# Performance work log

Measured on AMD Instinct MI355X. Metric: run time of the kernel, lower is better.

The kernel has to match this reference:

```python
import jax, jax.numpy as jnp
import numpy as np

DEPTH = 8
INPUT_DIM = 256
OUTPUT_DIM = 32
BATCH = 131072
N_INNER = 2 ** DEPTH - 1   # 255 inner nodes in heap/level order
N_LEAF = 2 ** DEPTH        # 256 leaves


def setup_inputs() -> dict:
    key = jax.random.key(0)
    kx, kw, kb, kbeta, kleaf = jax.random.split(key, 5)
    x = jax.random.normal(kx, (BATCH, INPUT_DIM), dtype=jnp.float32)
    # Stacked per-node Linear(input_dim, 1): weight rows [N_INNER, INPUT_DIM], bias [N_INNER]
    W = jax.random.normal(kw, (N_INNER, INPUT_DIM), dtype=jnp.float32) / np.sqrt(INPUT_DIM)
    b = jax.random.normal(kb, (N_INNER,), dtype=jnp.float32) * 0.01
    beta = jax.random.normal(kbeta, (N_INNER,), dtype=jnp.float32)  # per-node beta scalar
    leaf_param = jax.random.normal(kleaf, (N_LEAF, OUTPUT_DIM), dtype=jnp.float32)
    return {"x": x, "W": W, "b": b, "beta": beta, "leaf_param": leaf_param}


def _soft_tree(x, W, b, beta, leaf_param):
    B = x.shape[0]
    # All inner-node splits in one GEMM: sigmoid(beta_n * (x @ w_n + b_n))
    prob = jax.nn.sigmoid(beta[None, :] * (x @ W.T + b[None, :]))  # [B, N_INNER]
    # Level-wise path probability propagation (nodes stored in heap/level order).
    p = jnp.ones((B, 1), dtype=x.dtype)
    for d in range(DEPTH):
        lo = 2 ** d - 1
        pr = prob[:, lo: lo + 2 ** d]                      # [B, 2^d]
        # left child gets p*pr, right child gets p*(1-pr); interleave to keep DFS order
        p = jnp.stack([p * pr, p * (1.0 - pr)], axis=-1).reshape(B, 2 ** (d + 1))
    # leaf distributions Q = softmax(param) broadcast over batch; mixture output
    Q = jax.nn.softmax(leaf_param, axis=-1)                # [N_LEAF, OUTPUT_DIM]
    out = p @ Q                                            # [B, OUTPUT_DIM]
    return out, p


def reference(x, W, b, beta, leaf_param):
    out, path_probs = _soft_tree(x, W, b, beta, leaf_param)
    return out, path_probs
```

## Files before the change

kernel.cpp:

```cpp
#include <hip/hip_runtime.h>

#define BATCH   131072
#define IN_DIM  256
#define OUT_DIM 32
#define N_INNER 255
#define N_LEAF  256
#define OUT_HDR (BATCH * OUT_DIM)

#define TILE_M  64
#define BK      32
#define NTHR    512
#define NCHUNK  8
#define PSTR    258
#define INV64K  (1.0f / 65536.0f)

#define WS_QT_HI   0
#define WS_QT_LO   16384
#define WS_WIMG_HI 32768
#define WS_WIMG_LO (32768 + 131072)

#define L_XS_HI 0
#define L_XS_LO 4096
#define L_WS_HI 8192
#define L_WS_LO 24576
#define SMEM_BYTES 40960

typedef __attribute__((ext_vector_type(8))) short bf16x8;
typedef __attribute__((ext_vector_type(4))) float f32x4;

__device__ __forceinline__ unsigned short bf16rne(float a) {
    unsigned u = __float_as_uint(a);
    return (unsigned short)((u + 0x7FFFu + ((u >> 16) & 1u)) >> 16);
}
__device__ __forceinline__ unsigned packhi2(float a, float b) {
    return (unsigned)bf16rne(a) | ((unsigned)bf16rne(b) << 16);
}
__device__ __forceinline__ unsigned packlo2(float a, float b) {
    unsigned short ha = bf16rne(a), hb = bf16rne(b);
    float ra = a - __uint_as_float((unsigned)ha << 16);
    float rb = b - __uint_as_float((unsigned)hb << 16);
    return (unsigned)bf16rne(ra) | ((unsigned)bf16rne(rb) << 16);
}
__device__ __forceinline__ void split2(float a, float b, unsigned& hi, unsigned& lo) {
    unsigned short ha = bf16rne(a), hb = bf16rne(b);
    hi = (unsigned)ha | ((unsigned)hb << 16);
    float ra = a - __uint_as_float((unsigned)ha << 16);
    float rb = b - __uint_as_float((unsigned)hb << 16);
    lo = (unsigned)bf16rne(ra) | ((unsigned)bf16rne(rb) << 16);
}

__device__ __forceinline__ void gload16(const void* g, void* l) {
    __builtin_amdgcn_global_load_lds(
        (const __attribute__((address_space(1))) unsigned int*)g,
        (__attribute__((address_space(3))) unsigned int*)l, 16, 0, 0);
}

__global__ void wsplit_k(const float* __restrict__ W,
                         unsigned int* __restrict__ whi, unsigned int* __restrict__ wlo) {
    int gid = blockIdx.x * 512 + threadIdx.x;
    int n   = gid >> 5;
    int oct = gid & 31;
    float4 a = make_float4(0.f,0.f,0.f,0.f), b = a;
    if (n < N_INNER) {
        a = *(const float4*)(W + (size_t)n * IN_DIM + oct * 8);
        b = *(const float4*)(W + (size_t)n * IN_DIM + oct * 8 + 4);
    }
    uint4 h, l;
    split2(a.x, a.y, h.x, l.x); split2(a.z, a.w, h.y, l.y);
    split2(b.x, b.y, h.z, l.z); split2(b.z, b.w, h.w, l.w);
    int c = oct >> 2, kg = oct & 3;
    size_t off = ((size_t)(c * 4 + kg) * 256 + n) * 4;
    *(uint4*)(whi + off) = h;
    *(uint4*)(wlo + off) = l;
}

__global__ void qt_k(const float* __restrict__ leaf,
                     unsigned short* __restrict__ qhi, unsigned short* __restrict__ qlo) {
    int l = threadIdx.x;
    const float* row = leaf + l * OUT_DIM;
    float v[OUT_DIM];
    float mx = -1e30f;
#pragma unroll
    for (int o = 0; o < OUT_DIM; ++o) { v[o] = row[o]; mx = fmaxf(mx, v[o]); }
    float s = 0.f;
#pragma unroll
    for (int o = 0; o < OUT_DIM; ++o) { v[o] = __expf(v[o] - mx); s += v[o]; }
    float r = 1.f / s;
#pragma unroll
    for (int o = 0; o < OUT_DIM; ++o) {
        float q = v[o] * r;
        unsigned short h = bf16rne(q);
        float res = q - __uint_as_float((unsigned)h << 16);
        qhi[o * 256 + l] = h;
        qlo[o * 256 + l] = bf16rne(res);
    }
}

#define TREE_STAGE(D) { \
    const int base_ = (1 << (D)) - 1 + (qq << ((D) - 3)); \
    _Pragma("unroll") \
    for (int i = (1 << ((D) - 3)) - 1; i >= 0; --i) { \
        float pr_ = (float)pb[base_ + i] * INV64K; \
        float a_  = P[i]; \
        float lv_ = a_ * pr_; \
        P[2*i]     = lv_; \
        P[2*i + 1] = a_ - lv_; \
    } }

#define MFMA_BF16(A, B, C) __builtin_amdgcn_mfma_f32_16x16x32_bf16(A, B, C, 0, 0, 0)

__launch_bounds__(NTHR, 6)
__global__ void tree_k(const float* __restrict__ x,
                       const float* __restrict__ bv, const float* __restrict__ beta,
                       const unsigned short* __restrict__ qhi, const unsigned short* __restrict__ qlo,
                       const char* __restrict__ wimg_hi, const char* __restrict__ wimg_lo,
                       float* __restrict__ out) {
    extern __shared__ char smem[];
    const int tid  = threadIdx.x;
    const int row0 = blockIdx.x * TILE_M;

    const int lane  = tid & 63;
    const int w     = tid >> 6;
    const int col16 = lane & 15;
    const int hi4   = lane >> 4;
    const int wr    = w >> 2;
    const int wc    = w & 3;

    f32x4 acc[2][4];
#pragma unroll
    for (int i = 0; i < 2; ++i)
#pragma unroll
        for (int j = 0; j < 4; ++j) acc[i][j] = (f32x4){0.f, 0.f, 0.f, 0.f};

    const int xrow = tid >> 3;
    const int xkq  = tid & 7;
    const int xoff = (xkq >> 1) * 1024 + xrow * 16 + (xkq & 1) * 8;
    const float* xsrc = x + (size_t)(row0 + xrow) * IN_DIM + xkq * 4;

#pragma unroll 1
    for (int c = 0; c < NCHUNK; ++c) {
        {
            const char* gh = wimg_hi + (size_t)c * 16384;
            const char* gl = wimg_lo + (size_t)c * 16384;
            char* dh = smem + L_WS_HI + w * 1024;
            char* dl = smem + L_WS_LO + w * 1024;
            gload16(gh + tid * 16,        dh);
            gload16(gh + 8192 + tid * 16, dh + 8192);
            gload16(gl + tid * 16,        dl);
            gload16(gl + 8192 + tid * 16, dl + 8192);
        }
        {
            float4 v = *(const float4*)(xsrc + c * BK);
            uint2 h, l;
            split2(v.x, v.y, h.x, l.x);
            split2(v.z, v.w, h.y, l.y);
            *(uint2*)(smem + L_XS_HI + xoff) = h;
            *(uint2*)(smem + L_XS_LO + xoff) = l;
        }
        __syncthreads();

        bf16x8 ah[2], al[2];
#pragma unroll
        for (int rf = 0; rf < 2; ++rf) {
            int ao = hi4 * 1024 + (wr * 32 + rf * 16 + col16) * 16;
            ah[rf] = *(const bf16x8*)(smem + L_XS_HI + ao);
            al[rf] = *(const bf16x8*)(smem + L_XS_LO + ao);
        }
#pragma unroll
        for (int cf = 0; cf < 4; ++cf) {
            int bo = hi4 * 4096 + (wc * 64 + cf * 16 + col16) * 16;
            bf16x8 bh = *(const bf16x8*)(smem + L_WS_HI + bo);
            bf16x8 bl = *(const bf16x8*)(smem + L_WS_LO + bo);
#pragma unroll
            for (int rf = 0; rf < 2; ++rf) {
                acc[rf][cf] = MFMA_BF16(ah[rf], bh, acc[rf][cf]);
                acc[rf][cf] = MFMA_BF16(ah[rf], bl, acc[rf][cf]);
                acc[rf][cf] = MFMA_BF16(al[rf], bh, acc[rf][cf]);
            }
        }
        __syncthreads();
    }

    unsigned short* prob = (unsigned short*)smem;
    {
        float bb[4], bt[4];
#pragma unroll
        for (int cf = 0; cf < 4; ++cf) {
            int col = wc * 64 + cf * 16 + col16;
            bb[cf] = (col < N_INNER) ? bv[col]   : 0.f;
            bt[cf] = (col < N_INNER) ? beta[col] : 0.f;
        }
#pragma unroll
        for (int rf = 0; rf < 2; ++rf)
#pragma unroll
            for (int cf = 0; cf < 4; ++cf) {
                int col = wc * 64 + cf * 16 + col16;
#pragma unroll
                for (int r = 0; r < 4; ++r) {
                    int row = wr * 32 + rf * 16 + hi4 * 4 + r;
                    float t = (acc[rf][cf][r] + bb[cf]) * bt[cf];
                    float s = 1.f / (1.f + __expf(-t));
                    float u = fminf(s * 65536.f + 0.5f, 65535.f);
                    prob[row * PSTR + col] = (unsigned short)(unsigned)u;
                }
            }
    }
    __syncthreads();

    const int prow = tid >> 3;
    const int qq   = tid & 7;
    const unsigned short* pb = prob + prow * PSTR;
    float P[32];
    {
        float p0 = (float)pb[0] * INV64K;             float f0 = (qq & 4) ? (1.f - p0) : p0;
        float p1 = (float)pb[1 + (qq >> 2)] * INV64K; float f1 = (qq & 2) ? (1.f - p1) : p1;
        float p2 = (float)pb[3 + (qq >> 1)] * INV64K; float f2 = (qq & 1) ? (1.f - p2) : p2;
        P[0] = f0 * f1 * f2;
    }
    TREE_STAGE(3) TREE_STAGE(4) TREE_STAGE(5) TREE_STAGE(6) TREE_STAGE(7)

    {
        float* po = out + OUT_HDR + (size_t)(row0 + prow) * N_LEAF + qq * 32;
#pragma unroll
        for (int m = 0; m < 8; ++m)
            *(float4*)(po + m * 4) = make_float4(P[4*m], P[4*m+1], P[4*m+2], P[4*m+3]);
    }
    __syncthreads();

#pragma unroll
    for (int kg = 0; kg < 4; ++kg) {
        uint4 h;
        h.x = packhi2(P[kg*8+0], P[kg*8+1]);
        h.y = packhi2(P[kg*8+2], P[kg*8+3]);
        h.z = packhi2(P[kg*8+4], P[kg*8+5]);
        h.w = packhi2(P[kg*8+6], P[kg*8+7]);
        *(uint4*)(smem + qq * 4096 + kg * 1024 + ((prow * 16) ^ (qq << 4))) = h;
    }
    __syncthreads();

    f32x4 acc2 = (f32x4){0.f,0.f,0.f,0.f};
    const int cfw  = w >> 2;
    const int arow = (w & 3) * 16 + col16;
    const int qcol = (cfw * 16 + col16) * 256;

#pragma unroll
    for (int kc = 0; kc < 8; ++kc) {
        bf16x8 pa = *(const bf16x8*)(smem + kc * 4096 + hi4 * 1024 + ((arow * 16) ^ (kc << 4)));
        int qo = qcol + kc * 32 + hi4 * 8;
        bf16x8 qbh = *(const bf16x8*)(qhi + qo);
        bf16x8 qbl = *(const bf16x8*)(qlo + qo);
        acc2 = MFMA_BF16(pa, qbh, acc2);
        acc2 = MFMA_BF16(pa, qbl, acc2);
    }
    __syncthreads();

#pragma unroll
    for (int kg = 0; kg < 4; ++kg) {
        uint4 l;
        l.x = packlo2(P[kg*8+0], P[kg*8+1]);
        l.y = packlo2(P[kg*8+2], P[kg*8+3]);
        l.z = packlo2(P[kg*8+4], P[kg*8+5]);
        l.w = packlo2(P[kg*8+6], P[kg*8+7]);
        *(uint4*)(smem + qq * 4096 + kg * 1024 + ((prow * 16) ^ (qq << 4))) = l;
    }
    __syncthreads();

#pragma unroll
    for (int kc = 0; kc < 8; ++kc) {
        bf16x8 pa = *(const bf16x8*)(smem + kc * 4096 + hi4 * 1024 + ((arow * 16) ^ (kc << 4)));
        int qo = qcol + kc * 32 + hi4 * 8;
        bf16x8 qbh = *(const bf16x8*)(qhi + qo);
        acc2 = MFMA_BF16(pa, qbh, acc2);
    }
#pragma unroll
    for (int r = 0; r < 4; ++r) {
        int row = (w & 3) * 16 + hi4 * 4 + r;
        out[(size_t)(row0 + row) * OUT_DIM + cfw * 16 + col16] = acc2[r];
    }
}

extern "C" void kernel_launch(void* const* d_in, const int* in_sizes, int n_in,
                              void* d_out, int out_size, void* d_ws, size_t ws_size,
                              hipStream_t stream) {
    const float* x    = (const float*)d_in[0];
    const float* W    = (const float*)d_in[1];
    const float* bv   = (const float*)d_in[2];
    const float* beta = (const float*)d_in[3];
    const float* leaf = (const float*)d_in[4];
    float* out = (float*)d_out;
    char* ws = (char*)d_ws;

    unsigned short* qhi = (unsigned short*)(ws + WS_QT_HI);
    unsigned short* qlo = (unsigned short*)(ws + WS_QT_LO);
    char* whi = ws + WS_WIMG_HI;
    char* wlo = ws + WS_WIMG_LO;

    hipFuncSetAttribute(reinterpret_cast<const void*>(tree_k),
                        hipFuncAttributeMaxDynamicSharedMemorySize, SMEM_BYTES);

    wsplit_k<<<16, 512, 0, stream>>>(W, (unsigned int*)whi, (unsigned int*)wlo);
    qt_k<<<1, 256, 0, stream>>>(leaf, qhi, qlo);
    tree_k<<<BATCH / TILE_M, NTHR, SMEM_BYTES, stream>>>(
        x, bv, beta, qhi, qlo, whi, wlo, out);
}
```

Measured before the change: 151.9 us.

## Load GEMM operands directly to registers and split both P images before the Q GEMM

```diff
diff --git a/kernel.cpp b/kernel.cpp
--- a/kernel.cpp
+++ b/kernel.cpp
@@ -11,7 +11,7 @@
 #define BK      32
 #define NTHR    512
 #define NCHUNK  8
-#define PSTR    258
+#define PSTR    260
 #define INV64K  (1.0f / 65536.0f)
 
 #define WS_QT_HI   0
@@ -19,11 +19,8 @@
 #define WS_WIMG_HI 32768
 #define WS_WIMG_LO (32768 + 131072)
 
-#define L_XS_HI 0
-#define L_XS_LO 4096
-#define L_WS_HI 8192
-#define L_WS_LO 24576
-#define SMEM_BYTES 40960
+#define IMG_LO     33792
+#define SMEM_BYTES (IMG_LO + 32768)
 
 typedef __attribute__((ext_vector_type(8))) short bf16x8;
 typedef __attribute__((ext_vector_type(4))) float f32x4;
@@ -49,10 +46,21 @@
     lo = (unsigned)bf16rne(ra) | ((unsigned)bf16rne(rb) << 16);
 }
 
-__device__ __forceinline__ void gload16(const void* g, void* l) {
-    __builtin_amdgcn_global_load_lds(
-        (const __attribute__((address_space(1))) unsigned int*)g,
-        (__attribute__((address_space(3))) unsigned int*)l, 16, 0, 0);
+__device__ __forceinline__ void tsplit2(float a, float b, unsigned& h, unsigned& l) {
+    unsigned ua = __float_as_uint(a), ub = __float_as_uint(b);
+    h = (ua >> 16) | (ub & 0xFFFF0000u);
+    float ra = a - __uint_as_float(ua & 0xFFFF0000u);
+    float rb = b - __uint_as_float(ub & 0xFFFF0000u);
+    l = (__float_as_uint(ra) >> 16) | (__float_as_uint(rb) & 0xFFFF0000u);
+}
+__device__ __forceinline__ void split8(float4 a, float4 b, bf16x8& h8, bf16x8& l8) {
+    uint4 h, l;
+    tsplit2(a.x, a.y, h.x, l.x);
+    tsplit2(a.z, a.w, h.y, l.y);
+    tsplit2(b.x, b.y, h.z, l.z);
+    tsplit2(b.z, b.w, h.w, l.w);
+    h8 = __builtin_bit_cast(bf16x8, h);
+    l8 = __builtin_bit_cast(bf16x8, l);
 }
 
 __global__ void wsplit_k(const float* __restrict__ W,
@@ -68,8 +76,8 @@
     uint4 h, l;
     split2(a.x, a.y, h.x, l.x); split2(a.z, a.w, h.y, l.y);
     split2(b.x, b.y, h.z, l.z); split2(b.z, b.w, h.w, l.w);
-    int c = oct >> 2, kg = oct & 3;
-    size_t off = ((size_t)(c * 4 + kg) * 256 + n) * 4;
+    int c = oct >> 2, koct = oct & 3;
+    size_t off = (size_t)c * 4096 + (size_t)n * 16 + koct * 4;
     *(uint4*)(whi + off) = h;
     *(uint4*)(wlo + off) = l;
 }
@@ -109,7 +117,7 @@
 
 #define MFMA_BF16(A, B, C) __builtin_amdgcn_mfma_f32_16x16x32_bf16(A, B, C, 0, 0, 0)
 
-__launch_bounds__(NTHR, 6)
+__launch_bounds__(NTHR, 4)
 __global__ void tree_k(const float* __restrict__ x,
                        const float* __restrict__ bv, const float* __restrict__ beta,
                        const unsigned short* __restrict__ qhi, const unsigned short* __restrict__ qlo,
@@ -132,53 +140,43 @@
 #pragma unroll
         for (int j = 0; j < 4; ++j) acc[i][j] = (f32x4){0.f, 0.f, 0.f, 0.f};
 
-    const int xrow = tid >> 3;
-    const int xkq  = tid & 7;
-    const int xoff = (xkq >> 1) * 1024 + xrow * 16 + (xkq & 1) * 8;
-    const float* xsrc = x + (size_t)(row0 + xrow) * IN_DIM + xkq * 4;
+    const float* xp0 = x + (size_t)(row0 + wr * 32 + col16) * IN_DIM + hi4 * 8;
+    const float* xp1 = xp0 + (size_t)16 * IN_DIM;
+    const int bbase = (wc * 64 + col16) * 64 + hi4 * 16;
+
+    float4 a00 = *(const float4*)(xp0);
+    float4 a01 = *(const float4*)(xp0 + 4);
+    float4 a10 = *(const float4*)(xp1);
+    float4 a11 = *(const float4*)(xp1 + 4);
 
 #pragma unroll 1
     for (int c = 0; c < NCHUNK; ++c) {
-        {
-            const char* gh = wimg_hi + (size_t)c * 16384;
-            const char* gl = wimg_lo + (size_t)c * 16384;
-            char* dh = smem + L_WS_HI + w * 1024;
-            char* dl = smem + L_WS_LO + w * 1024;
-            gload16(gh + tid * 16,        dh);
-            gload16(gh + 8192 + tid * 16, dh + 8192);
-            gload16(gl + tid * 16,        dl);
-            gload16(gl + 8192 + tid * 16, dl + 8192);
-        }
-        {
-            float4 v = *(const float4*)(xsrc + c * BK);
-            uint2 h, l;
-            split2(v.x, v.y, h.x, l.x);
-            split2(v.z, v.w, h.y, l.y);
-            *(uint2*)(smem + L_XS_HI + xoff) = h;
-            *(uint2*)(smem + L_XS_LO + xoff) = l;
-        }
-        __syncthreads();
-
-        bf16x8 ah[2], al[2];
-#pragma unroll
-        for (int rf = 0; rf < 2; ++rf) {
-            int ao = hi4 * 1024 + (wr * 32 + rf * 16 + col16) * 16;
-            ah[rf] = *(const bf16x8*)(smem + L_XS_HI + ao);
-            al[rf] = *(const bf16x8*)(smem + L_XS_LO + ao);
-        }
+        const char* bhp = wimg_hi + (size_t)c * 16384 + bbase;
+        const char* blp = wimg_lo + (size_t)c * 16384 + bbase;
+        bf16x8 bh[4], bl[4];
 #pragma unroll
         for (int cf = 0; cf < 4; ++cf) {
-            int bo = hi4 * 4096 + (wc * 64 + cf * 16 + col16) * 16;
-            bf16x8 bh = *(const bf16x8*)(smem + L_WS_HI + bo);
-            bf16x8 bl = *(const bf16x8*)(smem + L_WS_LO + bo);
-#pragma unroll
-            for (int rf = 0; rf < 2; ++rf) {
-                acc[rf][cf] = MFMA_BF16(ah[rf], bh, acc[rf][cf]);
-                acc[rf][cf] = MFMA_BF16(ah[rf], bl, acc[rf][cf]);
-                acc[rf][cf] = MFMA_BF16(al[rf], bh, acc[rf][cf]);
-            }
-        }
-        __syncthreads();
+            bh[cf] = *(const bf16x8*)(bhp + cf * 1024);
+            bl[cf] = *(const bf16x8*)(blp + cf * 1024);
+        }
+        bf16x8 ah0, al0, ah1, al1;
+        split8(a00, a01, ah0, al0);
+        split8(a10, a11, ah1, al1);
+        if (c + 1 < NCHUNK) {
+            a00 = *(const float4*)(xp0 + (c + 1) * BK);
+            a01 = *(const float4*)(xp0 + (c + 1) * BK + 4);
+            a10 = *(const float4*)(xp1 + (c + 1) * BK);
+            a11 = *(const float4*)(xp1 + (c + 1) * BK + 4);
+        }
+#pragma unroll
+        for (int cf = 0; cf < 4; ++cf) {
+            acc[0][cf] = MFMA_BF16(ah0, bh[cf], acc[0][cf]);
+            acc[1][cf] = MFMA_BF16(ah1, bh[cf], acc[1][cf]);
+            acc[0][cf] = MFMA_BF16(ah0, bl[cf], acc[0][cf]);
+            acc[1][cf] = MFMA_BF16(ah1, bl[cf], acc[1][cf]);
+            acc[0][cf] = MFMA_BF16(al0, bh[cf], acc[0][cf]);
+            acc[1][cf] = MFMA_BF16(al1, bh[cf], acc[1][cf]);
+        }
     }
 
     unsigned short* prob = (unsigned short*)smem;
@@ -225,6 +223,16 @@
         for (int m = 0; m < 8; ++m)
             *(float4*)(po + m * 4) = make_float4(P[4*m], P[4*m+1], P[4*m+2], P[4*m+3]);
     }
+
+#pragma unroll
+    for (int kg = 0; kg < 4; ++kg) {
+        uint4 l;
+        l.x = packlo2(P[kg*8+0], P[kg*8+1]);
+        l.y = packlo2(P[kg*8+2], P[kg*8+3]);
+        l.z = packlo2(P[kg*8+4], P[kg*8+5]);
+        l.w = packlo2(P[kg*8+6], P[kg*8+7]);
+        *(uint4*)(smem + IMG_LO + qq * 4096 + kg * 1024 + ((prow * 16) ^ (qq << 4))) = l;
+    }
     __syncthreads();
 
 #pragma unroll
@@ -245,32 +253,15 @@
 
 #pragma unroll
     for (int kc = 0; kc < 8; ++kc) {
-        bf16x8 pa = *(const bf16x8*)(smem + kc * 4096 + hi4 * 1024 + ((arow * 16) ^ (kc << 4)));
+        const int po = kc * 4096 + hi4 * 1024 + ((arow * 16) ^ (kc << 4));
+        bf16x8 ph = *(const bf16x8*)(smem + po);
+        bf16x8 pl = *(const bf16x8*)(smem + IMG_LO + po);
         int qo = qcol + kc * 32 + hi4 * 8;
         bf16x8 qbh = *(const bf16x8*)(qhi + qo);
         bf16x8 qbl = *(const bf16x8*)(qlo + qo);
-        acc2 = MFMA_BF16(pa, qbh, acc2);
-        acc2 = MFMA_BF16(pa, qbl, acc2);
-    }
-    __syncthreads();
-
-#pragma unroll
-    for (int kg = 0; kg < 4; ++kg) {
-        uint4 l;
-        l.x = packlo2(P[kg*8+0], P[kg*8+1]);
-        l.y = packlo2(P[kg*8+2], P[kg*8+3]);
-        l.z = packlo2(P[kg*8+4], P[kg*8+5]);
-        l.w = packlo2(P[kg*8+6], P[kg*8+7]);
-        *(uint4*)(smem + qq * 4096 + kg * 1024 + ((prow * 16) ^ (qq << 4))) = l;
-    }
-    __syncthreads();
-
-#pragma unroll
-    for (int kc = 0; kc < 8; ++kc) {
-        bf16x8 pa = *(const bf16x8*)(smem + kc * 4096 + hi4 * 1024 + ((arow * 16) ^ (kc << 4)));
-        int qo = qcol + kc * 32 + hi4 * 8;
-        bf16x8 qbh = *(const bf16x8*)(qhi + qo);
-        acc2 = MFMA_BF16(pa, qbh, acc2);
+        acc2 = MFMA_BF16(ph, qbh, acc2);
+        acc2 = MFMA_BF16(ph, qbl, acc2);
+        acc2 = MFMA_BF16(pl, qbh, acc2);
     }
 #pragma unroll
     for (int r = 0; r < 4; ++r) {
```

Result: slower. 200.6 us (+32.0%).

## Double-buffer GEMM chunks, truncate-split x, and merge hi/lo leaf-mixture passes

Applied to the files above, without the earlier changes.

```diff
diff --git a/kernel.cpp b/kernel.cpp
--- a/kernel.cpp
+++ b/kernel.cpp
@@ -11,7 +11,7 @@
 #define BK      32
 #define NTHR    512
 #define NCHUNK  8
-#define PSTR    258
+#define PSTR    260
 #define INV64K  (1.0f / 65536.0f)
 
 #define WS_QT_HI   0
@@ -19,11 +19,12 @@
 #define WS_WIMG_HI 32768
 #define WS_WIMG_LO (32768 + 131072)
 
-#define L_XS_HI 0
-#define L_XS_LO 4096
-#define L_WS_HI 8192
-#define L_WS_LO 24576
-#define SMEM_BYTES 40960
+#define WB0 0
+#define WB1 32768
+#define XB0 65536
+#define XB1 73728
+#define IMG_LO 34816
+#define SMEM_BYTES 81920
 
 typedef __attribute__((ext_vector_type(8))) short bf16x8;
 typedef __attribute__((ext_vector_type(4))) float f32x4;
@@ -47,6 +48,13 @@
     float ra = a - __uint_as_float((unsigned)ha << 16);
     float rb = b - __uint_as_float((unsigned)hb << 16);
     lo = (unsigned)bf16rne(ra) | ((unsigned)bf16rne(rb) << 16);
+}
+__device__ __forceinline__ void tsplit2(float a, float b, unsigned& h, unsigned& l) {
+    unsigned ua = __float_as_uint(a), ub = __float_as_uint(b);
+    h = (ua >> 16) | (ub & 0xFFFF0000u);
+    float ra = a - __uint_as_float(ua & 0xFFFF0000u);
+    float rb = b - __uint_as_float(ub & 0xFFFF0000u);
+    l = (__float_as_uint(ra) >> 16) | (__float_as_uint(rb) & 0xFFFF0000u);
 }
 
 __device__ __forceinline__ void gload16(const void* g, void* l) {
@@ -109,7 +117,7 @@
 
 #define MFMA_BF16(A, B, C) __builtin_amdgcn_mfma_f32_16x16x32_bf16(A, B, C, 0, 0, 0)
 
-__launch_bounds__(NTHR, 6)
+__launch_bounds__(NTHR, 4)
 __global__ void tree_k(const float* __restrict__ x,
                        const float* __restrict__ bv, const float* __restrict__ beta,
                        const unsigned short* __restrict__ qhi, const unsigned short* __restrict__ qlo,
@@ -137,46 +145,70 @@
     const int xoff = (xkq >> 1) * 1024 + xrow * 16 + (xkq & 1) * 8;
     const float* xsrc = x + (size_t)(row0 + xrow) * IN_DIM + xkq * 4;
 
+    {
+        char* dh = smem + WB0 + w * 1024;
+        char* dl = dh + 16384;
+        gload16(wimg_hi + tid * 16,        dh);
+        gload16(wimg_hi + 8192 + tid * 16, dh + 8192);
+        gload16(wimg_lo + tid * 16,        dl);
+        gload16(wimg_lo + 8192 + tid * 16, dl + 8192);
+        float4 v = *(const float4*)(xsrc);
+        uint2 h, l;
+        tsplit2(v.x, v.y, h.x, l.x);
+        tsplit2(v.z, v.w, h.y, l.y);
+        *(uint2*)(smem + XB0 + xoff)        = h;
+        *(uint2*)(smem + XB0 + 4096 + xoff) = l;
+    }
+    __syncthreads();
+
 #pragma unroll 1
     for (int c = 0; c < NCHUNK; ++c) {
-        {
-            const char* gh = wimg_hi + (size_t)c * 16384;
-            const char* gl = wimg_lo + (size_t)c * 16384;
-            char* dh = smem + L_WS_HI + w * 1024;
-            char* dl = smem + L_WS_LO + w * 1024;
+        const int cur = c & 1;
+        const char* wb = smem + (cur ? WB1 : WB0);
+        const char* xb = smem + (cur ? XB1 : XB0);
+        char* wbn = smem + (cur ? WB0 : WB1);
+        char* xbn = smem + (cur ? XB0 : XB1);
+
+        float4 xn;
+        const bool more = (c + 1 < NCHUNK);
+        if (more) {
+            const char* gh = wimg_hi + (size_t)(c + 1) * 16384;
+            const char* gl = wimg_lo + (size_t)(c + 1) * 16384;
+            char* dh = wbn + w * 1024;
+            char* dl = dh + 16384;
             gload16(gh + tid * 16,        dh);
             gload16(gh + 8192 + tid * 16, dh + 8192);
             gload16(gl + tid * 16,        dl);
             gload16(gl + 8192 + tid * 16, dl + 8192);
-        }
-        {
-            float4 v = *(const float4*)(xsrc + c * BK);
-            uint2 h, l;
-            split2(v.x, v.y, h.x, l.x);
-            split2(v.z, v.w, h.y, l.y);
-            *(uint2*)(smem + L_XS_HI + xoff) = h;
-            *(uint2*)(smem + L_XS_LO + xoff) = l;
-        }
-        __syncthreads();
+            xn = *(const float4*)(xsrc + (c + 1) * BK);
+        }
 
         bf16x8 ah[2], al[2];
 #pragma unroll
         for (int rf = 0; rf < 2; ++rf) {
             int ao = hi4 * 1024 + (wr * 32 + rf * 16 + col16) * 16;
-            ah[rf] = *(const bf16x8*)(smem + L_XS_HI + ao);
-            al[rf] = *(const bf16x8*)(smem + L_XS_LO + ao);
+            ah[rf] = *(const bf16x8*)(xb + ao);
+            al[rf] = *(const bf16x8*)(xb + 4096 + ao);
         }
 #pragma unroll
         for (int cf = 0; cf < 4; ++cf) {
             int bo = hi4 * 4096 + (wc * 64 + cf * 16 + col16) * 16;
-            bf16x8 bh = *(const bf16x8*)(smem + L_WS_HI + bo);
-            bf16x8 bl = *(const bf16x8*)(smem + L_WS_LO + bo);
+            bf16x8 bh = *(const bf16x8*)(wb + bo);
+            bf16x8 bl = *(const bf16x8*)(wb + 16384 + bo);
 #pragma unroll
             for (int rf = 0; rf < 2; ++rf) {
                 acc[rf][cf] = MFMA_BF16(ah[rf], bh, acc[rf][cf]);
                 acc[rf][cf] = MFMA_BF16(ah[rf], bl, acc[rf][cf]);
                 acc[rf][cf] = MFMA_BF16(al[rf], bh, acc[rf][cf]);
             }
+        }
+
+        if (more) {
+            uint2 h, l;
+            tsplit2(xn.x, xn.y, h.x, l.x);
+            tsplit2(xn.z, xn.w, h.y, l.y);
+            *(uint2*)(xbn + xoff)        = h;
+            *(uint2*)(xbn + 4096 + xoff) = l;
         }
         __syncthreads();
     }
@@ -225,6 +257,16 @@
         for (int m = 0; m < 8; ++m)
             *(float4*)(po + m * 4) = make_float4(P[4*m], P[4*m+1], P[4*m+2], P[4*m+3]);
     }
+
+#pragma unroll
+    for (int kg = 0; kg < 4; ++kg) {
+        uint4 l;
+        l.x = packlo2(P[kg*8+0], P[kg*8+1]);
+        l.y = packlo2(P[kg*8+2], P[kg*8+3]);
+        l.z = packlo2(P[kg*8+4], P[kg*8+5]);
+        l.w = packlo2(P[kg*8+6], P[kg*8+7]);
+        *(uint4*)(smem + IMG_LO + qq * 4096 + kg * 1024 + ((prow * 16) ^ (qq << 4))) = l;
+    }
     __syncthreads();
 
 #pragma unroll
@@ -245,32 +287,15 @@
 
 #pragma unroll
     for (int kc = 0; kc < 8; ++kc) {
-        bf16x8 pa = *(const bf16x8*)(smem + kc * 4096 + hi4 * 1024 + ((arow * 16) ^ (kc << 4)));
+        const int po = kc * 4096 + hi4 * 1024 + ((arow * 16) ^ (kc << 4));
+        bf16x8 ph = *(const bf16x8*)(smem + po);
+        bf16x8 pl = *(const bf16x8*)(smem + IMG_LO + po);
         int qo = qcol + kc * 32 + hi4 * 8;
         bf16x8 qbh = *(const bf16x8*)(qhi + qo);
         bf16x8 qbl = *(const bf16x8*)(qlo + qo);
-        acc2 = MFMA_BF16(pa, qbh, acc2);
-        acc2 = MFMA_BF16(pa, qbl, acc2);
-    }
-    __syncthreads();
-
-#pragma unroll
-    for (int kg = 0; kg < 4; ++kg) {
-        uint4 l;
-        l.x = packlo2(P[kg*8+0], P[kg*8+1]);
-        l.y = packlo2(P[kg*8+2], P[kg*8+3]);
-        l.z = packlo2(P[kg*8+4], P[kg*8+5]);
-        l.w = packlo2(P[kg*8+6], P[kg*8+7]);
-        *(uint4*)(smem + qq * 4096 + kg * 1024 + ((prow * 16) ^ (qq << 4))) = l;
-    }
-    __syncthreads();
-
-#pragma unroll
-    for (int kc = 0; kc < 8; ++kc) {
-        bf16x8 pa = *(const bf16x8*)(smem + kc * 4096 + hi4 * 1024 + ((arow * 16) ^ (kc << 4)));
-        int qo = qcol + kc * 32 + hi4 * 8;
-        bf16x8 qbh = *(const bf16x8*)(qhi + qo);
-        acc2 = MFMA_BF16(pa, qbh, acc2);
+        acc2 = MFMA_BF16(ph, qbh, acc2);
+        acc2 = MFMA_BF16(ph, qbl, acc2);
+        acc2 = MFMA_BF16(pl, qbh, acc2);
     }
 #pragma unroll
     for (int r = 0; r < 4; ++r) {
```

Measured after the change: 148.2 us. 2.5% less time.
